# Kernel optimization log

Measured on AMD Instinct MI355X. Metric: run time of the kernel, lower is better.

## Reference

```python
import jax, jax.numpy as jnp
import numpy as np
import math

EPS = 1e-5
HEADS = 8

def _lin(x, w, b):
    return x @ w.T + b

def _ln(x, g, b):
    m = x.mean(-1, keepdims=True)
    v = ((x - m) ** 2).mean(-1, keepdims=True)
    return (x - m) / jnp.sqrt(v + EPS) * g + b

def _bn_eval(x, g, b):
    # BatchNorm1d eval with init running stats (mean=0, var=1)
    return x / jnp.sqrt(1.0 + EPS) * g[None, :, None] + b[None, :, None]

def _conv1d(x, w, b, pad):
    y = jax.lax.conv_general_dilated(x, w, (1,), [(pad, pad)],
                                     dimension_numbers=('NCH', 'OIH', 'NCH'))
    return y + b[None, :, None]

def _interp_linear(x, out_len):
    # F.interpolate(mode='linear', align_corners=False) on last axis
    L = x.shape[-1]
    src = (jnp.arange(out_len) + 0.5) * (L / out_len) - 0.5
    src = jnp.clip(src, 0.0, L - 1)
    i0 = jnp.floor(src).astype(jnp.int32)
    i1 = jnp.minimum(i0 + 1, L - 1)
    w = (src - i0).astype(x.dtype)
    return x[..., i0] * (1.0 - w) + x[..., i1] * w

def setup_inputs():
    key = jax.random.key(0)
    ks = iter(jax.random.split(key, 64))
    def nrm(shape, scale=0.02):
        return jax.random.normal(next(ks), shape, dtype=jnp.float32) * scale
    B, T, N, H, HOR, C = 2, 64, 2048, 128, 24, 32
    return dict(
        x=jax.random.normal(next(ks), (B, T, N), dtype=jnp.float32),
        tc_w=nrm((C, 1, 3), 0.2), tc_b=jnp.zeros((C,)), tc_bn_g=jnp.ones((C,)), tc_bn_b=jnp.zeros((C,)),
        fp_w=nrm((H, C * T)), fp_b=jnp.zeros((H,)), fp_ln_g=jnp.ones((H,)), fp_ln_b=jnp.zeros((H,)),
        q_w=nrm((H, H)), q_b=jnp.zeros((H,)),
        k_w=nrm((H, H)), k_b=jnp.zeros((H,)),
        v_w=nrm((H, H)), v_b=jnp.zeros((H,)),
        o_w=nrm((H, H)), o_b=jnp.zeros((H,)),
        adj=nrm((1, HEADS, N, N), 0.02),
        s0_w=nrm((H, H, 1), 0.05), s0_b=jnp.zeros((H,)), s0_bn_g=jnp.ones((H,)), s0_bn_b=jnp.zeros((H,)),
        s1_w=nrm((H, H, 2), 0.05), s1_b=jnp.zeros((H,)), s1_bn_g=jnp.ones((H,)), s1_bn_b=jnp.zeros((H,)),
        fusion_weight=jnp.ones((2,)),
        fu_w=nrm((H, H)), fu_b=jnp.zeros((H,)), fu_ln_g=jnp.ones((H,)), fu_ln_b=jnp.zeros((H,)),
        pr1_w=nrm((H, H)), pr1_b=jnp.zeros((H,)), pr_ln_g=jnp.ones((H,)), pr_ln_b=jnp.zeros((H,)),
        pr2_w=nrm((HOR, H)), pr2_b=jnp.zeros((HOR,)),
        rg_w=nrm((HOR, H)), rg_b=jnp.zeros((HOR,)),
    )

def _forward(x, tc_w, tc_b, tc_bn_g, tc_bn_b, fp_w, fp_b, fp_ln_g, fp_ln_b,
             q_w, q_b, k_w, k_b, v_w, v_b, o_w, o_b, adj,
             s0_w, s0_b, s0_bn_g, s0_bn_b, s1_w, s1_b, s1_bn_g, s1_bn_b,
             fusion_weight, fu_w, fu_b, fu_ln_g, fu_ln_b,
             pr1_w, pr1_b, pr_ln_g, pr_ln_b, pr2_w, pr2_b, rg_w, rg_b):
    B, T, N = x.shape
    H = q_w.shape[0]
    hd = H // HEADS
    x_last = x[:, -1, :]                                  # (B, N)
    # temporal conv over the window per node
    xt = x.transpose(0, 2, 1).reshape(B * N, 1, T)
    f = jax.nn.relu(_bn_eval(_conv1d(xt, tc_w, tc_b, 1), tc_bn_g, tc_bn_b))
    f = f.reshape(B, N, -1)                               # (B, N, 32*T)
    feats = jax.nn.relu(_ln(_lin(f, fp_w, fp_b), fp_ln_g, fp_ln_b))
    # adaptive graph attention with learnable adjacency bias
    q = _lin(feats, q_w, q_b).reshape(B, N, HEADS, hd)
    k = _lin(feats, k_w, k_b).reshape(B, N, HEADS, hd)
    v = _lin(feats, v_w, v_b).reshape(B, N, HEADS, hd)
    scores = jnp.einsum('bnhd,bmhd->bhnm', q, k) / math.sqrt(hd) + adj
    attn = jax.nn.softmax(scores, axis=-1)                # (B, HEADS, N, N)
    reg = jnp.float32(1e-4) * jnp.mean(jnp.abs(attn))
    go = jnp.einsum('bhnm,bmhd->bnhd', attn, v).reshape(B, N, H)
    gf = _lin(go, o_w, o_b)                               # (B, N, H)
    # multi-scale fusion (conv over node axis, kernels 1 and 2)
    xc = gf.transpose(0, 2, 1)                            # (B, H, N)
    f0 = jax.nn.relu(_bn_eval(_conv1d(xc, s0_w, s0_b, 0), s0_bn_g, s0_bn_b))
    f1 = jax.nn.relu(_bn_eval(_conv1d(xc, s1_w, s1_b, 1), s1_bn_g, s1_bn_b))  # (B,H,N+1)
    f1 = _interp_linear(f1, N)
    alpha = jax.nn.softmax(fusion_weight)
    fused = (alpha[0] * f0 + alpha[1] * f1).transpose(0, 2, 1)
    ff = jax.nn.relu(_ln(_lin(fused, fu_w, fu_b), fu_ln_g, fu_ln_b))
    # progressive prediction refinement
    h = jax.nn.relu(_ln(_lin(ff, pr1_w, pr1_b), pr_ln_g, pr_ln_b))
    preds = _lin(h, pr2_w, pr2_b)                         # (B, N, horizon)
    gates = jax.nn.sigmoid(_lin(ff, rg_w, rg_b))
    refined = gates * x_last[..., None] + (1.0 - gates) * preds
    return refined.transpose(0, 2, 1), reg                # (B, horizon, N), scalar

def reference(x, tc_w, tc_b, tc_bn_g, tc_bn_b, fp_w, fp_b, fp_ln_g, fp_ln_b,
              q_w, q_b, k_w, k_b, v_w, v_b, o_w, o_b, adj,
              s0_w, s0_b, s0_bn_g, s0_bn_b, s1_w, s1_b, s1_bn_g, s1_bn_b,
              fusion_weight, fu_w, fu_b, fu_ln_g, fu_ln_b,
              pr1_w, pr1_b, pr_ln_g, pr_ln_b, pr2_w, pr2_b, rg_w, rg_b):
    return _forward(x, tc_w, tc_b, tc_bn_g, tc_bn_b, fp_w, fp_b, fp_ln_g, fp_ln_b,
                    q_w, q_b, k_w, k_b, v_w, v_b, o_w, o_b, adj,
                    s0_w, s0_b, s0_bn_g, s0_bn_b, s1_w, s1_b, s1_bn_g, s1_bn_b,
                    fusion_weight, fu_w, fu_b, fu_ln_g, fu_ln_b,
                    pr1_w, pr1_b, pr_ln_g, pr_ln_b, pr2_w, pr2_b, rg_w, rg_b)
```

## Files before the change

kernel.cpp:

```cpp
#include <hip/hip_runtime.h>

using f32x4  = __attribute__((ext_vector_type(4))) float;
using bf16x8 = __attribute__((ext_vector_type(8))) short;

#define DEV static __device__ __forceinline__

DEV unsigned short f2bf(float f){
  unsigned u = __float_as_uint(f);
  unsigned r = (u + 0x7FFFu + ((u >> 16) & 1u)) >> 16;
  return (unsigned short)r;
}

DEV int vperm(int n){
  return (n & ~63) | (n & 32) | ((n & 0xC) << 1) | ((n & 0x10) >> 2) | (n & 3);
}

__global__ __launch_bounds__(256) void prep_conv_kernel(
    const float* __restrict__ fp_w, const float* __restrict__ q_w,
    const float* __restrict__ k_w, const float* __restrict__ v_w,
    const float* __restrict__ o_w, const float* __restrict__ s0_w,
    const float* __restrict__ s1_w, const float* __restrict__ fu_w,
    const float* __restrict__ pr1_w, const float* __restrict__ pr2_w,
    const float* __restrict__ rg_w,
    unsigned short* __restrict__ fpw_bf, unsigned short* __restrict__ wcat_bf,
    float* __restrict__ o_wT, float* __restrict__ fu_wT, float* __restrict__ pr1_wT,
    float* __restrict__ s0_wT, float* __restrict__ s1_wT0, float* __restrict__ s1_wT1,
    float* __restrict__ pr2_wT, float* __restrict__ rg_wT,
    const float* __restrict__ x, const float* __restrict__ tc_w,
    const float* __restrict__ tc_b, const float* __restrict__ bn_g,
    const float* __restrict__ bn_b, unsigned short* __restrict__ f){
  if (blockIdx.x < 512){
    int i = blockIdx.x * 256 + threadIdx.x;
    const int stride = 512 * 256;
    for (int idx = i; idx < 128 * 2048; idx += stride) fpw_bf[idx] = f2bf(fp_w[idx]);
    for (int idx = i; idx < 384 * 128; idx += stride){
      int c = idx >> 7, k = idx & 127;
      float v;
      if (c < 128)      v = q_w[c * 128 + k] * 0.25f;
      else if (c < 256) v = k_w[(c - 128) * 128 + k];
      else              v = v_w[(c - 256) * 128 + k];
      wcat_bf[idx] = f2bf(v);
    }
    for (int idx = i; idx < 128 * 128; idx += stride){
      int k = idx >> 7, c = idx & 127;
      o_wT[idx]   = o_w[c * 128 + k];
      fu_wT[idx]  = fu_w[c * 128 + k];
      pr1_wT[idx] = pr1_w[c * 128 + k];
      s0_wT[idx]  = s0_w[c * 128 + k];
      s1_wT0[idx] = s1_w[(c * 128 + k) * 2 + 0];
      s1_wT1[idx] = s1_w[(c * 128 + k) * 2 + 1];
    }
    for (int idx = i; idx < 128 * 24; idx += stride){
      int k = idx / 24, c = idx % 24;
      pr2_wT[idx] = pr2_w[c * 128 + k];
      rg_wT[idx]  = rg_w[c * 128 + k];
    }
  } else {
    int lane = threadIdx.x & 63;
    int w = threadIdx.x >> 6;
    int row = (blockIdx.x - 512) * 4 + w;
    int b = row >> 11, n = row & 2047;
    float xv = x[(size_t)(b * 64 + lane) * 2048 + n];
    float xm = __shfl_up(xv, 1, 64);   if (lane == 0)  xm = 0.f;
    float xp = __shfl_down(xv, 1, 64); if (lane == 63) xp = 0.f;
    const float inv = rsqrtf(1.0f + 1e-5f);
    unsigned short* frow = f + (size_t)row * 2048;
    #pragma unroll
    for (int c = 0; c < 32; c++){
      float y = xm * tc_w[c * 3 + 0] + xv * tc_w[c * 3 + 1] + xp * tc_w[c * 3 + 2] + tc_b[c];
      y = y * inv * bn_g[c] + bn_b[c];
      frow[c * 64 + lane] = f2bf(fmaxf(y, 0.f));
    }
  }
}

__global__ __launch_bounds__(512) void featqkv_kernel(
    const unsigned short* __restrict__ f, const unsigned short* __restrict__ fpw,
    const float* __restrict__ fp_b, const float* __restrict__ ln_g,
    const float* __restrict__ ln_b,
    const unsigned short* __restrict__ wcat, const float* __restrict__ q_b,
    const float* __restrict__ k_b, const float* __restrict__ v_b,
    unsigned short* __restrict__ qo, unsigned short* __restrict__ ko,
    unsigned short* __restrict__ vTp){
  __shared__ float pre[16][128];
  __shared__ unsigned short ft[16 * 128];
  __shared__ float stat[16][2];
  int t = threadIdx.x;
  int lane = t & 63, w = t >> 6;
  int l15 = lane & 15, g = lane >> 4;
  int row0 = blockIdx.x * 16;
  int b = row0 >> 11, n0 = row0 & 2047;
  int c0 = w * 16;
  f32x4 acc = {0.f,0.f,0.f,0.f};
  const unsigned short* arow = f   + (size_t)(row0 + l15) * 2048 + g * 8;
  const unsigned short* bp   = fpw + (size_t)(c0 + l15) * 2048 + g * 8;
  #pragma unroll 4
  for (int k = 0; k < 2048; k += 32){
    bf16x8 a  = *(const bf16x8*)(arow + k);
    bf16x8 b0 = *(const bf16x8*)(bp + k);
    acc = __builtin_amdgcn_mfma_f32_16x16x32_bf16(a, b0, acc, 0, 0, 0);
  }
  #pragma unroll
  for (int r = 0; r < 4; r++)
    pre[g * 4 + r][c0 + l15] = acc[r] + fp_b[c0 + l15];
  __syncthreads();
  if (t < 256){
    int r = t >> 4, j = t & 15;
    float s = 0.f, ss = 0.f;
    #pragma unroll
    for (int q = 0; q < 8; q++){ float v = pre[r][j + q * 16]; s += v; ss += v * v; }
    #pragma unroll
    for (int m = 1; m < 16; m <<= 1){ s += __shfl_xor(s, m, 64); ss += __shfl_xor(ss, m, 64); }
    if (j == 0){
      float mean = s * (1.f / 128.f);
      stat[r][0] = mean;
      stat[r][1] = rsqrtf(ss * (1.f / 128.f) - mean * mean + 1e-5f);
    }
  }
  __syncthreads();
  if (t < 256){
    int r = t >> 4, j = t & 15;
    float mean = stat[r][0], rstd = stat[r][1];
    bf16x8 outv;
    #pragma unroll
    for (int q = 0; q < 8; q++){
      int cc = j * 8 + q;
      float v = (pre[r][cc] - mean) * rstd * ln_g[cc] + ln_b[cc];
      outv[q] = (short)f2bf(fmaxf(v, 0.f));
    }
    int byte = r * 256 + ((j * 16) ^ ((r & 7) << 4));
    *(bf16x8*)((char*)ft + byte) = outv;
  }
  __syncthreads();
  f32x4 acc3[3] = {{0,0,0,0},{0,0,0,0},{0,0,0,0}};
  #pragma unroll
  for (int kk = 0; kk < 128; kk += 32){
    int abyte = l15 * 256 + (((kk + g * 8) * 2) ^ ((l15 & 7) << 4));
    bf16x8 a = *(const bf16x8*)((const char*)ft + abyte);
    #pragma unroll
    for (int ci = 0; ci < 3; ci++){
      int cc0 = w * 48 + ci * 16;
      bf16x8 bb = *(const bf16x8*)(wcat + (size_t)(cc0 + l15) * 128 + g * 8 + kk);
      acc3[ci] = __builtin_amdgcn_mfma_f32_16x16x32_bf16(a, bb, acc3[ci], 0, 0, 0);
    }
  }
  #pragma unroll
  for (int ci = 0; ci < 3; ci++){
    int c = w * 48 + ci * 16 + l15;
    int mat = c >> 7, cm = c & 127;
    int hh = cm >> 4, d = cm & 15;
    float bias = (mat == 0) ? q_b[cm] * 0.25f : (mat == 1 ? k_b[cm] : v_b[cm]);
    int bh = b * 8 + hh;
    #pragma unroll
    for (int r = 0; r < 4; r++){
      int n = n0 + g * 4 + r;
      unsigned short bv = f2bf(acc3[ci][r] + bias);
      if (mat == 0)      qo[((size_t)bh * 2048 + n) * 16 + d] = bv;
      else if (mat == 1) ko[((size_t)bh * 2048 + n) * 16 + d] = bv;
      else               vTp[((size_t)bh * 16 + d) * 2048 + vperm(n)] = bv;
    }
  }
}

__global__ __launch_bounds__(512) void attn_kernel(
    const unsigned short* __restrict__ qo, const unsigned short* __restrict__ ko,
    const unsigned short* __restrict__ vTp, const float* __restrict__ adj,
    float* __restrict__ go){
  __shared__ float red_acc[8][2][16][16];
  __shared__ float red_rs[8][2][16];
  int t = threadIdx.x, lane = t & 63, w = t >> 6;
  int l15 = lane & 15, g = lane >> 4;
  int h = blockIdx.x >> 7;
  int row0 = (blockIdx.x & 127) * 16;
  const bf16x8 zf = {0,0,0,0,0,0,0,0};
  const f32x4 z4 = {0.f,0.f,0.f,0.f};
  bf16x8 qf[2];
  #pragma unroll
  for (int b2 = 0; b2 < 2; b2++){
    if (g < 2) qf[b2] = *(const bf16x8*)(qo + ((size_t)(b2 * 8 + h) * 2048 + row0 + l15) * 16 + g * 8);
    else       qf[b2] = zf;
  }
  f32x4 accv[2] = {{0.f,0.f,0.f,0.f},{0.f,0.f,0.f,0.f}};
  float rsp[2] = {0.f, 0.f};
  const float* adjrow = adj + ((size_t)h * 2048 + row0 + l15) * 2048 + g * 4;
  const int mbeg = w * 256;
  for (int m0 = mbeg; m0 < mbeg + 256; m0 += 64){
    f32x4 adjv[4];
    #pragma unroll
    for (int s = 0; s < 4; s++)
      adjv[s] = *(const f32x4*)(adjrow + m0 + s * 16);
    #pragma unroll
    for (int b2 = 0; b2 < 2; b2++){
      int bh = b2 * 8 + h;
      const unsigned short* kbase = ko + (size_t)bh * 2048 * 16;
      f32x4 sf[4];
      #pragma unroll
      for (int s = 0; s < 4; s++){
        bf16x8 kf;
        if (g < 2) kf = *(const bf16x8*)(kbase + (size_t)(m0 + s * 16 + l15) * 16 + g * 8);
        else       kf = zf;
        sf[s] = __builtin_amdgcn_mfma_f32_16x16x32_bf16(kf, qf[b2], z4, 0, 0, 0);
      }
      bf16x8 pf[2];
      float partial = 0.f;
      #pragma unroll
      for (int s = 0; s < 4; s++){
        #pragma unroll
        for (int r = 0; r < 4; r++){
          float p = __expf(sf[s][r] + adjv[s][r]);
          partial += p;
          pf[s >> 1][(s & 1) * 4 + r] = (short)f2bf(p);
        }
      }
      rsp[b2] += partial;
      const unsigned short* vbase = vTp + ((size_t)bh * 16 + l15) * 2048 + m0;
      bf16x8 vf0 = *(const bf16x8*)(vbase + g * 8);
      bf16x8 vf1 = *(const bf16x8*)(vbase + 32 + g * 8);
      accv[b2] = __builtin_amdgcn_mfma_f32_16x16x32_bf16(vf0, pf[0], accv[b2], 0, 0, 0);
      accv[b2] = __builtin_amdgcn_mfma_f32_16x16x32_bf16(vf1, pf[1], accv[b2], 0, 0, 0);
    }
  }
  #pragma unroll
  for (int b2 = 0; b2 < 2; b2++){
    float s = rsp[b2];
    s += __shfl_xor(s, 16, 64);
    s += __shfl_xor(s, 32, 64);
    #pragma unroll
    for (int r = 0; r < 4; r++) red_acc[w][b2][g * 4 + r][l15] = accv[b2][r];
    if (lane < 16) red_rs[w][b2][l15] = s;
  }
  __syncthreads();
  {
    int b2 = t >> 8, qq = (t >> 4) & 15, d = t & 15;
    float v = 0.f, den = 0.f;
    #pragma unroll
    for (int ww = 0; ww < 8; ww++){ v += red_acc[ww][b2][d][qq]; den += red_rs[ww][b2][qq]; }
    go[((size_t)b2 * 2048 + row0 + qq) * 128 + h * 16 + d] = v / den;
  }
}

__global__ __launch_bounds__(512) void tail_kernel(
    const float* __restrict__ go, const float* __restrict__ x,
    const float* __restrict__ o_wT, const float* __restrict__ o_b,
    const float* __restrict__ s0_wT, const float* __restrict__ s0_b,
    const float* __restrict__ s0_g, const float* __restrict__ s0_bb,
    const float* __restrict__ s1_wT0, const float* __restrict__ s1_wT1,
    const float* __restrict__ s1_b, const float* __restrict__ s1_g,
    const float* __restrict__ s1_bb, const float* __restrict__ fw,
    const float* __restrict__ fu_wT, const float* __restrict__ fu_b,
    const float* __restrict__ fu_g, const float* __restrict__ fu_bb,
    const float* __restrict__ pr1_wT, const float* __restrict__ pr1_b,
    const float* __restrict__ pr_g, const float* __restrict__ pr_bb,
    const float* __restrict__ pr2_wT, const float* __restrict__ pr2_b,
    const float* __restrict__ rg_wT, const float* __restrict__ rg_b,
    float* __restrict__ out){
  __shared__ float go_s[20][128];
  __shared__ float gf_s[21][128];
  __shared__ float f1_s[17][128];
  __shared__ float fu_in[16][128];
  __shared__ float pre_s[16][128];
  __shared__ float ff_s[16][128];
  __shared__ float h_s[16][128];
  __shared__ float stat[16][2];
  int t = threadIdx.x;
  int b = blockIdx.x >> 7;
  int n0 = (blockIdx.x & 127) * 16;
  for (int e = t; e < 20 * 128; e += 512){
    int lr = e >> 7, cc = e & 127;
    int gn = n0 - 1 + lr;
    go_s[lr][cc] = (lr < 18 && gn >= 0 && gn < 2048) ? go[((size_t)b * 2048 + gn) * 128 + cc] : 0.f;
  }
  __syncthreads();
  int c = t & 127, q4 = t >> 7;
  const float bninv = rsqrtf(1.0f + 1e-5f);
  {
    float acc[5];
    float bias = o_b[c];
    #pragma unroll
    for (int i = 0; i < 5; i++) acc[i] = bias;
    for (int k = 0; k < 128; k++){
      float wv = o_wT[k * 128 + c];
      #pragma unroll
      for (int i = 0; i < 5; i++) acc[i] += go_s[i * 4 + q4][k] * wv;
    }
    #pragma unroll
    for (int i = 0; i < 5; i++){
      int lr = i * 4 + q4;
      int gn = n0 - 1 + lr;
      gf_s[lr][c] = (lr < 18 && gn >= 0 && gn < 2048) ? acc[i] : 0.f;
    }
    if (t < 128) gf_s[20][t] = 0.f;
  }
  __syncthreads();
  {
    float acc[5];
    float bias = s1_b[c];
    #pragma unroll
    for (int i = 0; i < 5; i++) acc[i] = bias;
    for (int k = 0; k < 128; k++){
      float w0 = s1_wT0[k * 128 + c], w1 = s1_wT1[k * 128 + c];
      #pragma unroll
      for (int i = 0; i < 5; i++)
        acc[i] += gf_s[i * 4 + q4][k] * w0 + gf_s[i * 4 + q4 + 1][k] * w1;
    }
    float sc = s1_g[c] * bninv, bb2 = s1_bb[c];
    #pragma unroll
    for (int i = 0; i < 5; i++){
      int lr = i * 4 + q4;
      if (lr < 17) f1_s[lr][c] = fmaxf(acc[i] * sc + bb2, 0.f);
    }
  }
  __syncthreads();
  {
    float acc[4];
    float bias = s0_b[c];
    #pragma unroll
    for (int i = 0; i < 4; i++) acc[i] = bias;
    for (int k = 0; k < 128; k++){
      float wv = s0_wT[k * 128 + c];
      #pragma unroll
      for (int i = 0; i < 4; i++) acc[i] += gf_s[i * 4 + q4 + 1][k] * wv;
    }
    float e0 = __expf(fw[0]), e1 = __expf(fw[1]);
    float a0 = e0 / (e0 + e1), a1 = e1 / (e0 + e1);
    float sc = s0_g[c] * bninv, bb2 = s0_bb[c];
    #pragma unroll
    for (int i = 0; i < 4; i++){
      int lr = i * 4 + q4;
      int n = n0 + lr;
      float f0 = fmaxf(acc[i] * sc + bb2, 0.f);
      float wn = (n + 0.5f) * (1.0f / 2048.0f);
      fu_in[lr][c] = a0 * f0 + a1 * ((1.f - wn) * f1_s[lr][c] + wn * f1_s[lr + 1][c]);
    }
  }
  __syncthreads();
  {
    float acc[4];
    float bias = fu_b[c];
    #pragma unroll
    for (int i = 0; i < 4; i++) acc[i] = bias;
    for (int k = 0; k < 128; k++){
      float wv = fu_wT[k * 128 + c];
      #pragma unroll
      for (int i = 0; i < 4; i++) acc[i] += fu_in[i * 4 + q4][k] * wv;
    }
    #pragma unroll
    for (int i = 0; i < 4; i++) pre_s[i * 4 + q4][c] = acc[i];
  }
  __syncthreads();
  if (t < 256){
    int r = t >> 4, j = t & 15;
    float s = 0.f, ss = 0.f;
    #pragma unroll
    for (int q = 0; q < 8; q++){ float v = pre_s[r][j + q * 16]; s += v; ss += v * v; }
    #pragma unroll
    for (int m = 1; m < 16; m <<= 1){ s += __shfl_xor(s, m, 64); ss += __shfl_xor(ss, m, 64); }
    if (j == 0){ float mean = s * (1.f / 128.f); stat[r][0] = mean;
                 stat[r][1] = rsqrtf(ss * (1.f / 128.f) - mean * mean + 1e-5f); }
  }
  __syncthreads();
  if (t < 256){
    int r = t >> 4, j = t & 15;
    float mean = stat[r][0], rstd = stat[r][1];
    #pragma unroll
    for (int q = 0; q < 8; q++){
      int cc = j * 8 + q;
      ff_s[r][cc] = fmaxf((pre_s[r][cc] - mean) * rstd * fu_g[cc] + fu_bb[cc], 0.f);
    }
  }
  __syncthreads();
  {
    float acc[4];
    float bias = pr1_b[c];
    #pragma unroll
    for (int i = 0; i < 4; i++) acc[i] = bias;
    for (int k = 0; k < 128; k++){
      float wv = pr1_wT[k * 128 + c];
      #pragma unroll
      for (int i = 0; i < 4; i++) acc[i] += ff_s[i * 4 + q4][k] * wv;
    }
    #pragma unroll
    for (int i = 0; i < 4; i++) pre_s[i * 4 + q4][c] = acc[i];
  }
  __syncthreads();
  if (t < 256){
    int r = t >> 4, j = t & 15;
    float s = 0.f, ss = 0.f;
    #pragma unroll
    for (int q = 0; q < 8; q++){ float v = pre_s[r][j + q * 16]; s += v; ss += v * v; }
    #pragma unroll
    for (int m = 1; m < 16; m <<= 1){ s += __shfl_xor(s, m, 64); ss += __shfl_xor(ss, m, 64); }
    if (j == 0){ float mean = s * (1.f / 128.f); stat[r][0] = mean;
                 stat[r][1] = rsqrtf(ss * (1.f / 128.f) - mean * mean + 1e-5f); }
  }
  __syncthreads();
  if (t < 256){
    int r = t >> 4, j = t & 15;
    float mean = stat[r][0], rstd = stat[r][1];
    #pragma unroll
    for (int q = 0; q < 8; q++){
      int cc = j * 8 + q;
      h_s[r][cc] = fmaxf((pre_s[r][cc] - mean) * rstd * pr_g[cc] + pr_bb[cc], 0.f);
    }
  }
  __syncthreads();
  if (t < 384){
    int lr = t / 24, cc = t % 24;
    float accp = pr2_b[cc], accg = rg_b[cc];
    for (int k = 0; k < 128; k++){
      accp += h_s[lr][k] * pr2_wT[k * 24 + cc];
      accg += ff_s[lr][k] * rg_wT[k * 24 + cc];
    }
    float gate = 1.f / (1.f + __expf(-accg));
    int n = n0 + lr;
    float xl = x[((size_t)b * 64 + 63) * 2048 + n];
    out[((size_t)b * 24 + cc) * 2048 + n] = gate * xl + (1.f - gate) * accp;
  }
  if (blockIdx.x == 0 && t == 0) out[2 * 24 * 2048] = 1e-4f / 2048.0f;
}

extern "C" void kernel_launch(void* const* d_in, const int* in_sizes, int n_in,
                              void* d_out, int out_size, void* d_ws, size_t ws_size,
                              hipStream_t stream){
  const float* x       = (const float*)d_in[0];
  const float* tc_w    = (const float*)d_in[1];
  const float* tc_b    = (const float*)d_in[2];
  const float* tc_bn_g = (const float*)d_in[3];
  const float* tc_bn_b = (const float*)d_in[4];
  const float* fp_w    = (const float*)d_in[5];
  const float* fp_b    = (const float*)d_in[6];
  const float* fp_ln_g = (const float*)d_in[7];
  const float* fp_ln_b = (const float*)d_in[8];
  const float* q_w     = (const float*)d_in[9];
  const float* q_b     = (const float*)d_in[10];
  const float* k_w     = (const float*)d_in[11];
  const float* k_b     = (const float*)d_in[12];
  const float* v_w     = (const float*)d_in[13];
  const float* v_b     = (const float*)d_in[14];
  const float* o_w     = (const float*)d_in[15];
  const float* o_b     = (const float*)d_in[16];
  const float* adj     = (const float*)d_in[17];
  const float* s0_w    = (const float*)d_in[18];
  const float* s0_b    = (const float*)d_in[19];
  const float* s0_bn_g = (const float*)d_in[20];
  const float* s0_bn_b = (const float*)d_in[21];
  const float* s1_w    = (const float*)d_in[22];
  const float* s1_b    = (const float*)d_in[23];
  const float* s1_bn_g = (const float*)d_in[24];
  const float* s1_bn_b = (const float*)d_in[25];
  const float* fusion_w= (const float*)d_in[26];
  const float* fu_w    = (const float*)d_in[27];
  const float* fu_b    = (const float*)d_in[28];
  const float* fu_ln_g = (const float*)d_in[29];
  const float* fu_ln_b = (const float*)d_in[30];
  const float* pr1_w   = (const float*)d_in[31];
  const float* pr1_b   = (const float*)d_in[32];
  const float* pr_ln_g = (const float*)d_in[33];
  const float* pr_ln_b = (const float*)d_in[34];
  const float* pr2_w   = (const float*)d_in[35];
  const float* pr2_b   = (const float*)d_in[36];
  const float* rg_w    = (const float*)d_in[37];
  const float* rg_b    = (const float*)d_in[38];
  float* out = (float*)d_out;

  char* ws = (char*)d_ws;
  size_t off = 0;
  auto alloc = [&](size_t bytes) -> void* {
    void* p = ws + off;
    off += (bytes + 255) & ~(size_t)255;
    return p;
  };
  unsigned short* f_bf    = (unsigned short*)alloc((size_t)4096 * 2048 * 2);
  unsigned short* fpw_bf  = (unsigned short*)alloc((size_t)128 * 2048 * 2);
  unsigned short* wcat_bf = (unsigned short*)alloc((size_t)384 * 128 * 2);
  unsigned short* q_bf    = (unsigned short*)alloc((size_t)16 * 2048 * 16 * 2);
  unsigned short* k_bf    = (unsigned short*)alloc((size_t)16 * 2048 * 16 * 2);
  unsigned short* vTp_bf  = (unsigned short*)alloc((size_t)16 * 2048 * 16 * 2);
  float* go     = (float*)alloc((size_t)4096 * 128 * 4);
  float* o_wT   = (float*)alloc(128 * 128 * 4);
  float* fu_wT  = (float*)alloc(128 * 128 * 4);
  float* pr1_wT = (float*)alloc(128 * 128 * 4);
  float* s0_wT  = (float*)alloc(128 * 128 * 4);
  float* s1_wT0 = (float*)alloc(128 * 128 * 4);
  float* s1_wT1 = (float*)alloc(128 * 128 * 4);
  float* pr2_wT = (float*)alloc(128 * 24 * 4);
  float* rg_wT  = (float*)alloc(128 * 24 * 4);
  if (off > ws_size) return;

  prep_conv_kernel<<<1536, 256, 0, stream>>>(fp_w, q_w, k_w, v_w, o_w, s0_w, s1_w,
                                             fu_w, pr1_w, pr2_w, rg_w, fpw_bf, wcat_bf,
                                             o_wT, fu_wT, pr1_wT, s0_wT, s1_wT0, s1_wT1,
                                             pr2_wT, rg_wT,
                                             x, tc_w, tc_b, tc_bn_g, tc_bn_b, f_bf);
  featqkv_kernel<<<256, 512, 0, stream>>>(f_bf, fpw_bf, fp_b, fp_ln_g, fp_ln_b,
                                          wcat_bf, q_b, k_b, v_b, q_bf, k_bf, vTp_bf);
  attn_kernel<<<1024, 512, 0, stream>>>(q_bf, k_bf, vTp_bf, adj, go);
  tail_kernel<<<256, 512, 0, stream>>>(go, x, o_wT, o_b, s0_wT, s0_b, s0_bn_g, s0_bn_b,
                                       s1_wT0, s1_wT1, s1_b, s1_bn_g, s1_bn_b, fusion_w,
                                       fu_wT, fu_b, fu_ln_g, fu_ln_b, pr1_wT, pr1_b,
                                       pr_ln_g, pr_ln_b, pr2_wT, pr2_b, rg_wT, rg_b, out);
}
```

Measured before the change: 134.1 us.

## Fuse temporal conv into feature projection GEMM via swizzled LDS tiles

Moves the conv1d+BN+ReLU feature generation out of the prep kernel and into the feature-projection GEMM kernel. Each block loads its 64x16 slice of x into shared memory and computes the bf16 features for two 16-channel halves into a XOR-swizzled LDS tile, which the MFMA loop then consumes. This removes the 16 MB bf16 intermediate write and read through global memory, and the weight prep kernel shrinks to 128 blocks. In exchange the GEMM kernel uses more shared memory (~40KB per 512-thread block), adds extra barriers, and now spends compute on the conv before its MFMA work.

```diff
diff --git a/kernel.cpp b/kernel.cpp
--- a/kernel.cpp
+++ b/kernel.cpp
@@ -15,7 +15,7 @@
   return (n & ~63) | (n & 32) | ((n & 0xC) << 1) | ((n & 0x10) >> 2) | (n & 3);
 }
 
-__global__ __launch_bounds__(256) void prep_conv_kernel(
+__global__ __launch_bounds__(256) void prep_kernel(
     const float* __restrict__ fp_w, const float* __restrict__ q_w,
     const float* __restrict__ k_w, const float* __restrict__ v_w,
     const float* __restrict__ o_w, const float* __restrict__ s0_w,
@@ -25,63 +25,46 @@
     unsigned short* __restrict__ fpw_bf, unsigned short* __restrict__ wcat_bf,
     float* __restrict__ o_wT, float* __restrict__ fu_wT, float* __restrict__ pr1_wT,
     float* __restrict__ s0_wT, float* __restrict__ s1_wT0, float* __restrict__ s1_wT1,
-    float* __restrict__ pr2_wT, float* __restrict__ rg_wT,
+    float* __restrict__ pr2_wT, float* __restrict__ rg_wT){
+  int i = blockIdx.x * 256 + threadIdx.x;
+  const int stride = 128 * 256;
+  for (int idx = i; idx < 128 * 2048; idx += stride) fpw_bf[idx] = f2bf(fp_w[idx]);
+  for (int idx = i; idx < 384 * 128; idx += stride){
+    int c = idx >> 7, k = idx & 127;
+    float v;
+    if (c < 128)      v = q_w[c * 128 + k] * 0.25f;
+    else if (c < 256) v = k_w[(c - 128) * 128 + k];
+    else              v = v_w[(c - 256) * 128 + k];
+    wcat_bf[idx] = f2bf(v);
+  }
+  for (int idx = i; idx < 128 * 128; idx += stride){
+    int k = idx >> 7, c = idx & 127;
+    o_wT[idx]   = o_w[c * 128 + k];
+    fu_wT[idx]  = fu_w[c * 128 + k];
+    pr1_wT[idx] = pr1_w[c * 128 + k];
+    s0_wT[idx]  = s0_w[c * 128 + k];
+    s1_wT0[idx] = s1_w[(c * 128 + k) * 2 + 0];
+    s1_wT1[idx] = s1_w[(c * 128 + k) * 2 + 1];
+  }
+  for (int idx = i; idx < 128 * 24; idx += stride){
+    int k = idx / 24, c = idx % 24;
+    pr2_wT[idx] = pr2_w[c * 128 + k];
+    rg_wT[idx]  = rg_w[c * 128 + k];
+  }
+}
+
+__global__ __launch_bounds__(512) void convfeatqkv_kernel(
     const float* __restrict__ x, const float* __restrict__ tc_w,
     const float* __restrict__ tc_b, const float* __restrict__ bn_g,
-    const float* __restrict__ bn_b, unsigned short* __restrict__ f){
-  if (blockIdx.x < 512){
-    int i = blockIdx.x * 256 + threadIdx.x;
-    const int stride = 512 * 256;
-    for (int idx = i; idx < 128 * 2048; idx += stride) fpw_bf[idx] = f2bf(fp_w[idx]);
-    for (int idx = i; idx < 384 * 128; idx += stride){
-      int c = idx >> 7, k = idx & 127;
-      float v;
-      if (c < 128)      v = q_w[c * 128 + k] * 0.25f;
-      else if (c < 256) v = k_w[(c - 128) * 128 + k];
-      else              v = v_w[(c - 256) * 128 + k];
-      wcat_bf[idx] = f2bf(v);
-    }
-    for (int idx = i; idx < 128 * 128; idx += stride){
-      int k = idx >> 7, c = idx & 127;
-      o_wT[idx]   = o_w[c * 128 + k];
-      fu_wT[idx]  = fu_w[c * 128 + k];
-      pr1_wT[idx] = pr1_w[c * 128 + k];
-      s0_wT[idx]  = s0_w[c * 128 + k];
-      s1_wT0[idx] = s1_w[(c * 128 + k) * 2 + 0];
-      s1_wT1[idx] = s1_w[(c * 128 + k) * 2 + 1];
-    }
-    for (int idx = i; idx < 128 * 24; idx += stride){
-      int k = idx / 24, c = idx % 24;
-      pr2_wT[idx] = pr2_w[c * 128 + k];
-      rg_wT[idx]  = rg_w[c * 128 + k];
-    }
-  } else {
-    int lane = threadIdx.x & 63;
-    int w = threadIdx.x >> 6;
-    int row = (blockIdx.x - 512) * 4 + w;
-    int b = row >> 11, n = row & 2047;
-    float xv = x[(size_t)(b * 64 + lane) * 2048 + n];
-    float xm = __shfl_up(xv, 1, 64);   if (lane == 0)  xm = 0.f;
-    float xp = __shfl_down(xv, 1, 64); if (lane == 63) xp = 0.f;
-    const float inv = rsqrtf(1.0f + 1e-5f);
-    unsigned short* frow = f + (size_t)row * 2048;
-    #pragma unroll
-    for (int c = 0; c < 32; c++){
-      float y = xm * tc_w[c * 3 + 0] + xv * tc_w[c * 3 + 1] + xp * tc_w[c * 3 + 2] + tc_b[c];
-      y = y * inv * bn_g[c] + bn_b[c];
-      frow[c * 64 + lane] = f2bf(fmaxf(y, 0.f));
-    }
-  }
-}
-
-__global__ __launch_bounds__(512) void featqkv_kernel(
-    const unsigned short* __restrict__ f, const unsigned short* __restrict__ fpw,
-    const float* __restrict__ fp_b, const float* __restrict__ ln_g,
-    const float* __restrict__ ln_b,
+    const float* __restrict__ bn_b,
+    const unsigned short* __restrict__ fpw, const float* __restrict__ fp_b,
+    const float* __restrict__ ln_g, const float* __restrict__ ln_b,
     const unsigned short* __restrict__ wcat, const float* __restrict__ q_b,
     const float* __restrict__ k_b, const float* __restrict__ v_b,
     unsigned short* __restrict__ qo, unsigned short* __restrict__ ko,
     unsigned short* __restrict__ vTp){
+  __shared__ float xs[64][17];
+  __shared__ unsigned short fs[16 * 1024];
   __shared__ float pre[16][128];
   __shared__ unsigned short ft[16 * 128];
   __shared__ float stat[16][2];
@@ -90,15 +73,52 @@
   int l15 = lane & 15, g = lane >> 4;
   int row0 = blockIdx.x * 16;
   int b = row0 >> 11, n0 = row0 & 2047;
+  const float bninv = rsqrtf(1.0f + 1e-5f);
+  for (int e = t; e < 1024; e += 512){
+    int tt = e >> 4, nn2 = e & 15;
+    xs[tt][nn2] = x[(size_t)(b * 64 + tt) * 2048 + n0 + nn2];
+  }
+  __syncthreads();
+  int nn = t & 15, chl = (t >> 4) & 15, th = t >> 8;
   int c0 = w * 16;
   f32x4 acc = {0.f,0.f,0.f,0.f};
-  const unsigned short* arow = f   + (size_t)(row0 + l15) * 2048 + g * 8;
-  const unsigned short* bp   = fpw + (size_t)(c0 + l15) * 2048 + g * 8;
-  #pragma unroll 4
-  for (int k = 0; k < 2048; k += 32){
-    bf16x8 a  = *(const bf16x8*)(arow + k);
-    bf16x8 b0 = *(const bf16x8*)(bp + k);
-    acc = __builtin_amdgcn_mfma_f32_16x16x32_bf16(a, b0, acc, 0, 0, 0);
+  const unsigned short* bp = fpw + (size_t)(c0 + l15) * 2048 + g * 8;
+  const char* fsbase = (const char*)fs + l15 * 2048;
+  int aswz = (l15 & 7) << 4;
+  char* fsrow = (char*)fs + nn * 2048;
+  int wswz = (nn & 7) << 4;
+  for (int half = 0; half < 2; half++){
+    {
+      int ch = half * 16 + chl;
+      float cw0 = tc_w[ch * 3 + 0], cw1 = tc_w[ch * 3 + 1], cw2 = tc_w[ch * 3 + 2];
+      float cb = tc_b[ch];
+      float csc = bninv * bn_g[ch], cbb = bn_b[ch];
+      int t0 = th * 32;
+      float xprev = (t0 > 0) ? xs[t0 - 1][nn] : 0.f;
+      float xcur  = xs[t0][nn];
+      #pragma unroll
+      for (int j = 0; j < 4; j++){
+        bf16x8 pack;
+        #pragma unroll
+        for (int i2 = 0; i2 < 8; i2++){
+          int tt = t0 + j * 8 + i2;
+          float xnext = (tt < 63) ? xs[tt + 1][nn] : 0.f;
+          float y = (xprev * cw0 + xcur * cw1 + xnext * cw2 + cb) * csc + cbb;
+          pack[i2] = (short)f2bf(fmaxf(y, 0.f));
+          xprev = xcur; xcur = xnext;
+        }
+        int kl = chl * 64 + t0 + j * 8;
+        *(bf16x8*)(fsrow + ((kl * 2) ^ wswz)) = pack;
+      }
+    }
+    __syncthreads();
+    #pragma unroll 4
+    for (int kk = 0; kk < 1024; kk += 32){
+      bf16x8 a  = *(const bf16x8*)(fsbase + (((kk + g * 8) * 2) ^ aswz));
+      bf16x8 b0 = *(const bf16x8*)(bp + half * 1024 + kk);
+      acc = __builtin_amdgcn_mfma_f32_16x16x32_bf16(a, b0, acc, 0, 0, 0);
+    }
+    __syncthreads();
   }
   #pragma unroll
   for (int r = 0; r < 4; r++)
@@ -470,7 +490,6 @@
     off += (bytes + 255) & ~(size_t)255;
     return p;
   };
-  unsigned short* f_bf    = (unsigned short*)alloc((size_t)4096 * 2048 * 2);
   unsigned short* fpw_bf  = (unsigned short*)alloc((size_t)128 * 2048 * 2);
   unsigned short* wcat_bf = (unsigned short*)alloc((size_t)384 * 128 * 2);
   unsigned short* q_bf    = (unsigned short*)alloc((size_t)16 * 2048 * 16 * 2);
@@ -487,13 +506,14 @@
   float* rg_wT  = (float*)alloc(128 * 24 * 4);
   if (off > ws_size) return;
 
-  prep_conv_kernel<<<1536, 256, 0, stream>>>(fp_w, q_w, k_w, v_w, o_w, s0_w, s1_w,
-                                             fu_w, pr1_w, pr2_w, rg_w, fpw_bf, wcat_bf,
-                                             o_wT, fu_wT, pr1_wT, s0_wT, s1_wT0, s1_wT1,
-                                             pr2_wT, rg_wT,
-                                             x, tc_w, tc_b, tc_bn_g, tc_bn_b, f_bf);
-  featqkv_kernel<<<256, 512, 0, stream>>>(f_bf, fpw_bf, fp_b, fp_ln_g, fp_ln_b,
-                                          wcat_bf, q_b, k_b, v_b, q_bf, k_bf, vTp_bf);
+  prep_kernel<<<128, 256, 0, stream>>>(fp_w, q_w, k_w, v_w, o_w, s0_w, s1_w,
+                                       fu_w, pr1_w, pr2_w, rg_w, fpw_bf, wcat_bf,
+                                       o_wT, fu_wT, pr1_wT, s0_wT, s1_wT0, s1_wT1,
+                                       pr2_wT, rg_wT);
+  convfeatqkv_kernel<<<256, 512, 0, stream>>>(x, tc_w, tc_b, tc_bn_g, tc_bn_b,
+                                              fpw_bf, fp_b, fp_ln_g, fp_ln_b,
+                                              wcat_bf, q_b, k_b, v_b,
+                                              q_bf, k_bf, vTp_bf);
   attn_kernel<<<1024, 512, 0, stream>>>(q_bf, k_bf, vTp_bf, adj, go);
   tail_kernel<<<256, 512, 0, stream>>>(go, x, o_wT, o_b, s0_wT, s0_b, s0_bn_g, s0_bn_b,
                                        s1_wT0, s1_wT1, s1_b, s1_bn_g, s1_bn_b, fusion_w,
```

Result: faster. 124.1 us (-7.4%).
